# Optimization experiments

Hardware: AMD Instinct MI355X
Metric: run time of the kernel (lower is better)

## Reference

```python
import jax, jax.numpy as jnp
import numpy as np


def _combine(left, right):
    # complex mult-add combine: (a_r, x_r) o (a_l, x_l) = (a_r*a_l, a_r*x_l + x_r)
    alr, ali, xlr, xli = left
    arr, ari, xrr, xri = right
    rar = arr * alr - ari * ali
    rai = arr * ali + ari * alr
    rxr = arr * xlr - ari * xli + xrr
    rxi = arr * xli + ari * xlr + xri
    return (rar, rai, rxr, rxi)


def setup_inputs() -> dict:
    key = jax.random.key(0)
    k1, k2, k3, k4 = jax.random.split(key, 4)
    B, L, D = 8, 4096, 256
    A_re = jax.random.uniform(k1, (B, L, D), dtype=jnp.float32)  # |a|<1-ish for stability
    A_im = jax.random.normal(k2, (B, L, D), dtype=jnp.float32) * 0.1
    X_re = jax.random.normal(k3, (B, L, D), dtype=jnp.float32)
    X_im = jax.random.normal(k4, (B, L, D), dtype=jnp.float32)
    return {"A_re": A_re, "A_im": A_im, "X_re": X_re, "X_im": X_im}


def reference(A_re, A_im, X_re, X_im):
    # Inclusive scan of y_t = a_t * y_{t-1} + x_t (complex), over time axis 1.
    _, _, yr, yi = jax.lax.associative_scan(_combine, (A_re, A_im, X_re, X_im), axis=1)
    # [B, L, D, 2] real/imag stacked (equivalent of torch.view_as_real of the complex output)
    return jnp.stack([yr, yi], axis=-1)
```

## Files before the change

kernel.cpp:

```cpp
#include <hip/hip_runtime.h>

#define BATCH 8
#define SEQ   4096
#define DIM   256

typedef float floatx4 __attribute__((ext_vector_type(4)));


template <int NT, int T>
__global__ __launch_bounds__(256) void k_tile_agg(
    const float* __restrict__ Ar, const float* __restrict__ Ai,
    const float* __restrict__ Xr, const float* __restrict__ Xi,
    float4* __restrict__ agg)
{
    int wave = threadIdx.x >> 6;
    int lane = threadIdx.x & 63;
    int tile = blockIdx.x * 4 + wave;
    int b = tile / NT;
    int j = tile - b * NT;
    int d = lane * 4;

    size_t base = ((size_t)b * SEQ + (size_t)j * T) * DIM + d;

    float pr[4], pi[4], yr[4], yi[4];
#pragma unroll
    for (int k = 0; k < 4; ++k) { pr[k] = 1.f; pi[k] = 0.f; yr[k] = 0.f; yi[k] = 0.f; }

#pragma unroll 4
    for (int t = 0; t < T; ++t) {
        size_t idx = base + (size_t)t * DIM;
        float4 a_re = *(const float4*)(Ar + idx);
        float4 a_im = *(const float4*)(Ai + idx);
        float4 x_re = *(const float4*)(Xr + idx);
        float4 x_im = *(const float4*)(Xi + idx);
        const float* par = (const float*)&a_re;
        const float* pai = (const float*)&a_im;
        const float* pxr = (const float*)&x_re;
        const float* pxi = (const float*)&x_im;
#pragma unroll
        for (int k = 0; k < 4; ++k) {
            float a_r = par[k], a_i = pai[k];
            float npr = a_r * pr[k] - a_i * pi[k];
            float npi = a_r * pi[k] + a_i * pr[k];
            pr[k] = npr; pi[k] = npi;
            float nyr = a_r * yr[k] - a_i * yi[k] + pxr[k];
            float nyi = a_r * yi[k] + a_i * yr[k] + pxi[k];
            yr[k] = nyr; yi[k] = nyi;
        }
    }

    size_t o = ((size_t)b * NT + j) * DIM + d;
#pragma unroll
    for (int k = 0; k < 4; ++k)
        agg[o + k] = make_float4(pr[k], pi[k], yr[k], yi[k]);
}

template <int NT>
__global__ __launch_bounds__(256) void k_scan_agg(float4* __restrict__ agg)
{
    constexpr int NTPL = NT / 64;
    int lane = threadIdx.x & 63;
    int col  = blockIdx.x * 4 + (threadIdx.x >> 6);
    int b = col >> 8;
    int d = col & 255;

    float4 v[NTPL];
    float lar = 1.f, lai = 0.f, lxr = 0.f, lxi = 0.f;
#pragma unroll
    for (int m = 0; m < NTPL; ++m) {
        v[m] = agg[((size_t)b * NT + lane * NTPL + m) * DIM + d];
        float nar = v[m].x * lar - v[m].y * lai;
        float nai = v[m].x * lai + v[m].y * lar;
        float nxr = v[m].x * lxr - v[m].y * lxi + v[m].z;
        float nxi = v[m].x * lxi + v[m].y * lxr + v[m].w;
        lar = nar; lai = nai; lxr = nxr; lxi = nxi;
    }

    float ar = lar, ai = lai, xr = lxr, xi = lxi;
#pragma unroll
    for (int off = 1; off < 64; off <<= 1) {
        float par = __shfl_up(ar, (unsigned)off, 64);
        float pai = __shfl_up(ai, (unsigned)off, 64);
        float pxr = __shfl_up(xr, (unsigned)off, 64);
        float pxi = __shfl_up(xi, (unsigned)off, 64);
        if (lane >= off) {
            float nar = ar * par - ai * pai;
            float nai = ar * pai + ai * par;
            float nxr = ar * pxr - ai * pxi + xr;
            float nxi = ar * pxi + ai * pxr + xi;
            ar = nar; ai = nai; xr = nxr; xi = nxi;
        }
    }

    float ear = __shfl_up(ar, 1u, 64);
    float eai = __shfl_up(ai, 1u, 64);
    float exr = __shfl_up(xr, 1u, 64);
    float exi = __shfl_up(xi, 1u, 64);
    if (lane == 0) { ear = 1.f; eai = 0.f; exr = 0.f; exi = 0.f; }

#pragma unroll
    for (int m = 0; m < NTPL; ++m) {
        agg[((size_t)b * NT + lane * NTPL + m) * DIM + d] =
            make_float4(exr, exi, 0.f, 0.f);
        float nar = v[m].x * ear - v[m].y * eai;
        float nai = v[m].x * eai + v[m].y * ear;
        float nxr = v[m].x * exr - v[m].y * exi + v[m].z;
        float nxi = v[m].x * exi + v[m].y * exr + v[m].w;
        ear = nar; eai = nai; exr = nxr; exi = nxi;
    }
}

template <int NT, int T>
__global__ __launch_bounds__(256, 8) void k_apply(
    const float* __restrict__ Ar, const float* __restrict__ Ai,
    const float* __restrict__ Xr, const float* __restrict__ Xi,
    const float4* __restrict__ agg, float* __restrict__ outf)
{
    int half = threadIdx.x >> 7;
    int wl   = threadIdx.x & 127;
    int tile = blockIdx.x * 2 + half;
    int b = tile / NT;
    int j = tile - b * NT;
    int d = wl * 2;

    float yr[2], yi[2];
    size_t o = ((size_t)b * NT + j) * DIM + d;
    {
        float4 p0 = agg[o];
        float4 p1 = agg[o + 1];
        yr[0] = p0.x; yi[0] = p0.y;
        yr[1] = p1.x; yi[1] = p1.y;
    }

    size_t base = ((size_t)b * SEQ + (size_t)j * T) * DIM + d;

#pragma unroll
    for (int t = 0; t < T; ++t) {
        size_t idx = base + (size_t)t * DIM;
        float2 a_re = *(const float2*)(Ar + idx);
        float2 a_im = *(const float2*)(Ai + idx);
        float2 x_re = *(const float2*)(Xr + idx);
        float2 x_im = *(const float2*)(Xi + idx);
        const float* par = (const float*)&a_re;
        const float* pai = (const float*)&a_im;
        const float* pxr = (const float*)&x_re;
        const float* pxi = (const float*)&x_im;
#pragma unroll
        for (int k = 0; k < 2; ++k) {
            float nyr = par[k] * yr[k] - pai[k] * yi[k] + pxr[k];
            float nyi = par[k] * yi[k] + pai[k] * yr[k] + pxi[k];
            yr[k] = nyr; yi[k] = nyi;
        }
        floatx4 o1 = (floatx4){yr[0], yi[0], yr[1], yi[1]};
        __builtin_nontemporal_store(o1, (floatx4*)(outf + 2 * idx));
    }
}

extern "C" void kernel_launch(void* const* d_in, const int* in_sizes, int n_in,
                              void* d_out, int out_size, void* d_ws, size_t ws_size,
                              hipStream_t stream)
{
    const float* Ar = (const float*)d_in[0];
    const float* Ai = (const float*)d_in[1];
    const float* Xr = (const float*)d_in[2];
    const float* Xi = (const float*)d_in[3];
    float* outf = (float*)d_out;
    float4* agg = (float4*)d_ws;

    dim3 block(256);

    if (ws_size >= (size_t)BATCH * 256 * DIM * sizeof(float4)) {
        constexpr int NT = 256, T = SEQ / 256;
        dim3 grid1((BATCH * NT) / 4);
        dim3 grid3((BATCH * NT) / 2);
        k_tile_agg<NT, T><<<grid1, block, 0, stream>>>(Ar, Ai, Xr, Xi, agg);
        k_scan_agg<NT><<<(BATCH * DIM) / 4, block, 0, stream>>>(agg);
        k_apply<NT, T><<<grid3, block, 0, stream>>>(Ar, Ai, Xr, Xi, agg, outf);
    } else {
        constexpr int NT = 64, T = SEQ / 64;
        dim3 grid1((BATCH * NT) / 4);
        dim3 grid3((BATCH * NT) / 2);
        k_tile_agg<NT, T><<<grid1, block, 0, stream>>>(Ar, Ai, Xr, Xi, agg);
        k_scan_agg<NT><<<(BATCH * DIM) / 4, block, 0, stream>>>(agg);
        k_apply<NT, T><<<grid3, block, 0, stream>>>(Ar, Ai, Xr, Xi, agg, outf);
    }
}
```

Before: 67.90 us.

## Stage tile inputs into LDS via async global_load_lds in aggregation pass

Replaces the first-pass tile aggregation kernel with one that uses one block per tile. Each wave copies one of the four input arrays for the tile into LDS with direct global-to-LDS loads, then each thread scans one channel out of LDS. The goal is more memory-level parallelism and better coalescing in the bandwidth-bound aggregation pass. The cost is 64KB of LDS per block (T=16), which limits occupancy, plus a full barrier before any compute starts.

```diff
diff --git a/kernel.cpp b/kernel.cpp
--- a/kernel.cpp
+++ b/kernel.cpp
@@ -6,6 +6,57 @@
 
 typedef float floatx4 __attribute__((ext_vector_type(4)));
 
+
+template <int NT, int T>
+__global__ __launch_bounds__(256) void k_tile_agg_lds(
+    const float* __restrict__ Ar, const float* __restrict__ Ai,
+    const float* __restrict__ Xr, const float* __restrict__ Xi,
+    float4* __restrict__ agg)
+{
+    constexpr int TILE_FLOATS = T * DIM;
+    __shared__ float lds[4 * TILE_FLOATS];
+
+    int tile = blockIdx.x;
+    int b = tile / NT;
+    int j = tile - b * NT;
+
+    int wave = threadIdx.x >> 6;
+    int lane = threadIdx.x & 63;
+
+    size_t tile_off = ((size_t)b * SEQ + (size_t)j * T) * DIM;
+
+    const float* src = (wave == 0) ? Ar : (wave == 1) ? Ai
+                      : (wave == 2) ? Xr : Xi;
+    const float* gsrc = src + tile_off + (size_t)lane * 4;
+    float* lbase = &lds[wave * TILE_FLOATS];
+
+#pragma unroll
+    for (int s = 0; s < T; ++s) {
+        __builtin_amdgcn_global_load_lds(
+            (const __attribute__((address_space(1))) void*)(gsrc + s * DIM),
+            (__attribute__((address_space(3))) void*)(lbase + s * DIM),
+            16, 0, 0);
+    }
+    __syncthreads();
+
+    int d = threadIdx.x;
+    float pr = 1.f, pi = 0.f, yr = 0.f, yi = 0.f;
+#pragma unroll
+    for (int t = 0; t < T; ++t) {
+        float a_r = lds[0 * TILE_FLOATS + t * DIM + d];
+        float a_i = lds[1 * TILE_FLOATS + t * DIM + d];
+        float x_r = lds[2 * TILE_FLOATS + t * DIM + d];
+        float x_i = lds[3 * TILE_FLOATS + t * DIM + d];
+        float npr = a_r * pr - a_i * pi;
+        float npi = a_r * pi + a_i * pr;
+        pr = npr; pi = npi;
+        float nyr = a_r * yr - a_i * yi + x_r;
+        float nyi = a_r * yi + a_i * yr + x_i;
+        yr = nyr; yi = nyi;
+    }
+
+    agg[((size_t)b * NT + j) * DIM + d] = make_float4(pr, pi, yr, yi);
+}
 
 template <int NT, int T>
 __global__ __launch_bounds__(256) void k_tile_agg(
@@ -171,9 +222,9 @@
 
     if (ws_size >= (size_t)BATCH * 256 * DIM * sizeof(float4)) {
         constexpr int NT = 256, T = SEQ / 256;
-        dim3 grid1((BATCH * NT) / 4);
+        dim3 grid1(BATCH * NT);
         dim3 grid3((BATCH * NT) / 2);
-        k_tile_agg<NT, T><<<grid1, block, 0, stream>>>(Ar, Ai, Xr, Xi, agg);
+        k_tile_agg_lds<NT, T><<<grid1, block, 0, stream>>>(Ar, Ai, Xr, Xi, agg);
         k_scan_agg<NT><<<(BATCH * DIM) / 4, block, 0, stream>>>(agg);
         k_apply<NT, T><<<grid3, block, 0, stream>>>(Ar, Ai, Xr, Xi, agg, outf);
     } else {
```

After: 66.74 us. No clear change (-1.7%).

## Pipeline tile aggregation through LDS with double-buffered async global-to-LDS loads

Applied to the files above, without the earlier changes.

Replaces the first-pass tile aggregation kernel with a version that streams 8-timestep sub-tiles into LDS via global_load_lds, one wave per input array, double-buffered with explicit vmcnt waits and barriers. Each thread then computes the complex scan for one channel from LDS and writes an aggregate every two sub-tiles (16 steps, matching NT=256). The goal is to keep more memory requests in flight and overlap loading with the serial recurrence. In exchange it adds block-wide barriers, relies on precise vmcnt accounting, and uses 64KB of LDS per block, which limits occupancy.

```diff
diff --git a/kernel.cpp b/kernel.cpp
--- a/kernel.cpp
+++ b/kernel.cpp
@@ -6,6 +6,177 @@
 
 typedef float floatx4 __attribute__((ext_vector_type(4)));
 
+constexpr int NT_MAIN = 256;
+constexpr int T_MAIN  = SEQ / NT_MAIN;
+constexpr int TSUB    = 8;
+constexpr int SUB_FLOATS = TSUB * DIM;
+constexpr int NSUB_BLK   = 8;
+constexpr int NSUB_TOT   = BATCH * SEQ / TSUB;
+
+__global__ __launch_bounds__(256, 2) void k_tile_agg_pipe(
+    const float* __restrict__ Ar, const float* __restrict__ Ai,
+    const float* __restrict__ Xr, const float* __restrict__ Xi,
+    float4* __restrict__ agg)
+{
+    __shared__ float lds[2][4][SUB_FLOATS];
+
+    int wave = threadIdx.x >> 6, lane = threadIdx.x & 63;
+    int d = threadIdx.x;
+    const float* src = (wave == 0) ? Ar : (wave == 1) ? Ai
+                      : (wave == 2) ? Xr : Xi;
+
+    int s0 = blockIdx.x * NSUB_BLK;
+    const float* gsrc = src + (size_t)s0 * SUB_FLOATS + (size_t)lane * 4;
+
+    auto ISSUE = [&](int i) {
+        const float* g = gsrc + (size_t)i * SUB_FLOATS;
+        float* l = &lds[i & 1][wave][0];
+#pragma unroll
+        for (int r = 0; r < TSUB; ++r) {
+            __builtin_amdgcn_global_load_lds(
+                (const __attribute__((address_space(1))) void*)(g + r * DIM),
+                (__attribute__((address_space(3))) void*)(l + r * DIM),
+                16, 0, 0);
+        }
+    };
+
+    float pr = 1.f, pi = 0.f, yr = 0.f, yi = 0.f;
+
+    ISSUE(0);
+#pragma unroll 1
+    for (int i = 0; i < NSUB_BLK; ++i) {
+        if (i + 1 < NSUB_BLK) {
+            ISSUE(i + 1);
+            asm volatile("s_waitcnt vmcnt(8)" ::: "memory");
+        } else {
+            asm volatile("s_waitcnt vmcnt(0)" ::: "memory");
+        }
+        __builtin_amdgcn_s_barrier();
+        __builtin_amdgcn_sched_barrier(0);
+
+        const int buf = i & 1;
+#pragma unroll
+        for (int t = 0; t < TSUB; ++t) {
+            float a_r = lds[buf][0][t * DIM + d];
+            float a_i = lds[buf][1][t * DIM + d];
+            float x_r = lds[buf][2][t * DIM + d];
+            float x_i = lds[buf][3][t * DIM + d];
+            float npr = a_r * pr - a_i * pi;
+            float npi = a_r * pi + a_i * pr;
+            pr = npr; pi = npi;
+            float nyr = a_r * yr - a_i * yi + x_r;
+            float nyi = a_r * yi + a_i * yr + x_i;
+            yr = nyr; yi = nyi;
+        }
+        if (i & 1) {
+            int s = s0 + i;
+            agg[(size_t)(s >> 1) * DIM + d] = make_float4(pr, pi, yr, yi);
+            pr = 1.f; pi = 0.f; yr = 0.f; yi = 0.f;
+        }
+        __builtin_amdgcn_s_barrier();
+    }
+}
+
+template <int NT>
+__global__ __launch_bounds__(256) void k_scan_agg(float4* __restrict__ agg)
+{
+    constexpr int NTPL = NT / 64;
+    int lane = threadIdx.x & 63;
+    int col  = blockIdx.x * 4 + (threadIdx.x >> 6);
+    int b = col >> 8;
+    int d = col & 255;
+
+    float4 v[NTPL];
+    float lar = 1.f, lai = 0.f, lxr = 0.f, lxi = 0.f;
+#pragma unroll
+    for (int m = 0; m < NTPL; ++m) {
+        v[m] = agg[((size_t)b * NT + lane * NTPL + m) * DIM + d];
+        float nar = v[m].x * lar - v[m].y * lai;
+        float nai = v[m].x * lai + v[m].y * lar;
+        float nxr = v[m].x * lxr - v[m].y * lxi + v[m].z;
+        float nxi = v[m].x * lxi + v[m].y * lxr + v[m].w;
+        lar = nar; lai = nai; lxr = nxr; lxi = nxi;
+    }
+
+    float ar = lar, ai = lai, xr = lxr, xi = lxi;
+#pragma unroll
+    for (int off = 1; off < 64; off <<= 1) {
+        float par = __shfl_up(ar, (unsigned)off, 64);
+        float pai = __shfl_up(ai, (unsigned)off, 64);
+        float pxr = __shfl_up(xr, (unsigned)off, 64);
+        float pxi = __shfl_up(xi, (unsigned)off, 64);
+        if (lane >= off) {
+            float nar = ar * par - ai * pai;
+            float nai = ar * pai + ai * par;
+            float nxr = ar * pxr - ai * pxi + xr;
+            float nxi = ar * pxi + ai * pxr + xi;
+            ar = nar; ai = nai; xr = nxr; xi = nxi;
+        }
+    }
+
+    float ear = __shfl_up(ar, 1u, 64);
+    float eai = __shfl_up(ai, 1u, 64);
+    float exr = __shfl_up(xr, 1u, 64);
+    float exi = __shfl_up(xi, 1u, 64);
+    if (lane == 0) { ear = 1.f; eai = 0.f; exr = 0.f; exi = 0.f; }
+
+#pragma unroll
+    for (int m = 0; m < NTPL; ++m) {
+        agg[((size_t)b * NT + lane * NTPL + m) * DIM + d] =
+            make_float4(exr, exi, 0.f, 0.f);
+        float nar = v[m].x * ear - v[m].y * eai;
+        float nai = v[m].x * eai + v[m].y * ear;
+        float nxr = v[m].x * exr - v[m].y * exi + v[m].z;
+        float nxi = v[m].x * exi + v[m].y * exr + v[m].w;
+        ear = nar; eai = nai; exr = nxr; exi = nxi;
+    }
+}
+
+template <int NT, int T>
+__global__ __launch_bounds__(256, 8) void k_apply(
+    const float* __restrict__ Ar, const float* __restrict__ Ai,
+    const float* __restrict__ Xr, const float* __restrict__ Xi,
+    const float4* __restrict__ agg, float* __restrict__ outf)
+{
+    int half = threadIdx.x >> 7;
+    int wl   = threadIdx.x & 127;
+    int tile = blockIdx.x * 2 + half;
+    int b = tile / NT;
+    int j = tile - b * NT;
+    int d = wl * 2;
+
+    float yr[2], yi[2];
+    size_t o = ((size_t)b * NT + j) * DIM + d;
+    {
+        float4 p0 = agg[o];
+        float4 p1 = agg[o + 1];
+        yr[0] = p0.x; yi[0] = p0.y;
+        yr[1] = p1.x; yi[1] = p1.y;
+    }
+
+    size_t base = ((size_t)b * SEQ + (size_t)j * T) * DIM + d;
+
+#pragma unroll
+    for (int t = 0; t < T; ++t) {
+        size_t idx = base + (size_t)t * DIM;
+        float2 a_re = *(const float2*)(Ar + idx);
+        float2 a_im = *(const float2*)(Ai + idx);
+        float2 x_re = *(const float2*)(Xr + idx);
+        float2 x_im = *(const float2*)(Xi + idx);
+        const float* par = (const float*)&a_re;
+        const float* pai = (const float*)&a_im;
+        const float* pxr = (const float*)&x_re;
+        const float* pxi = (const float*)&x_im;
+#pragma unroll
+        for (int k = 0; k < 2; ++k) {
+            float nyr = par[k] * yr[k] - pai[k] * yi[k] + pxr[k];
+            float nyi = par[k] * yi[k] + pai[k] * yr[k] + pxi[k];
+            yr[k] = nyr; yi[k] = nyi;
+        }
+        floatx4 o1 = (floatx4){yr[0], yi[0], yr[1], yi[1]};
+        __builtin_nontemporal_store(o1, (floatx4*)(outf + 2 * idx));
+    }
+}
 
 template <int NT, int T>
 __global__ __launch_bounds__(256) void k_tile_agg(
@@ -55,107 +226,6 @@
         agg[o + k] = make_float4(pr[k], pi[k], yr[k], yi[k]);
 }
 
-template <int NT>
-__global__ __launch_bounds__(256) void k_scan_agg(float4* __restrict__ agg)
-{
-    constexpr int NTPL = NT / 64;
-    int lane = threadIdx.x & 63;
-    int col  = blockIdx.x * 4 + (threadIdx.x >> 6);
-    int b = col >> 8;
-    int d = col & 255;
-
-    float4 v[NTPL];
-    float lar = 1.f, lai = 0.f, lxr = 0.f, lxi = 0.f;
-#pragma unroll
-    for (int m = 0; m < NTPL; ++m) {
-        v[m] = agg[((size_t)b * NT + lane * NTPL + m) * DIM + d];
-        float nar = v[m].x * lar - v[m].y * lai;
-        float nai = v[m].x * lai + v[m].y * lar;
-        float nxr = v[m].x * lxr - v[m].y * lxi + v[m].z;
-        float nxi = v[m].x * lxi + v[m].y * lxr + v[m].w;
-        lar = nar; lai = nai; lxr = nxr; lxi = nxi;
-    }
-
-    float ar = lar, ai = lai, xr = lxr, xi = lxi;
-#pragma unroll
-    for (int off = 1; off < 64; off <<= 1) {
-        float par = __shfl_up(ar, (unsigned)off, 64);
-        float pai = __shfl_up(ai, (unsigned)off, 64);
-        float pxr = __shfl_up(xr, (unsigned)off, 64);
-        float pxi = __shfl_up(xi, (unsigned)off, 64);
-        if (lane >= off) {
-            float nar = ar * par - ai * pai;
-            float nai = ar * pai + ai * par;
-            float nxr = ar * pxr - ai * pxi + xr;
-            float nxi = ar * pxi + ai * pxr + xi;
-            ar = nar; ai = nai; xr = nxr; xi = nxi;
-        }
-    }
-
-    float ear = __shfl_up(ar, 1u, 64);
-    float eai = __shfl_up(ai, 1u, 64);
-    float exr = __shfl_up(xr, 1u, 64);
-    float exi = __shfl_up(xi, 1u, 64);
-    if (lane == 0) { ear = 1.f; eai = 0.f; exr = 0.f; exi = 0.f; }
-
-#pragma unroll
-    for (int m = 0; m < NTPL; ++m) {
-        agg[((size_t)b * NT + lane * NTPL + m) * DIM + d] =
-            make_float4(exr, exi, 0.f, 0.f);
-        float nar = v[m].x * ear - v[m].y * eai;
-        float nai = v[m].x * eai + v[m].y * ear;
-        float nxr = v[m].x * exr - v[m].y * exi + v[m].z;
-        float nxi = v[m].x * exi + v[m].y * exr + v[m].w;
-        ear = nar; eai = nai; exr = nxr; exi = nxi;
-    }
-}
-
-template <int NT, int T>
-__global__ __launch_bounds__(256, 8) void k_apply(
-    const float* __restrict__ Ar, const float* __restrict__ Ai,
-    const float* __restrict__ Xr, const float* __restrict__ Xi,
-    const float4* __restrict__ agg, float* __restrict__ outf)
-{
-    int half = threadIdx.x >> 7;
-    int wl   = threadIdx.x & 127;
-    int tile = blockIdx.x * 2 + half;
-    int b = tile / NT;
-    int j = tile - b * NT;
-    int d = wl * 2;
-
-    float yr[2], yi[2];
-    size_t o = ((size_t)b * NT + j) * DIM + d;
-    {
-        float4 p0 = agg[o];
-        float4 p1 = agg[o + 1];
-        yr[0] = p0.x; yi[0] = p0.y;
-        yr[1] = p1.x; yi[1] = p1.y;
-    }
-
-    size_t base = ((size_t)b * SEQ + (size_t)j * T) * DIM + d;
-
-#pragma unroll
-    for (int t = 0; t < T; ++t) {
-        size_t idx = base + (size_t)t * DIM;
-        float2 a_re = *(const float2*)(Ar + idx);
-        float2 a_im = *(const float2*)(Ai + idx);
-        float2 x_re = *(const float2*)(Xr + idx);
-        float2 x_im = *(const float2*)(Xi + idx);
-        const float* par = (const float*)&a_re;
-        const float* pai = (const float*)&a_im;
-        const float* pxr = (const float*)&x_re;
-        const float* pxi = (const float*)&x_im;
-#pragma unroll
-        for (int k = 0; k < 2; ++k) {
-            float nyr = par[k] * yr[k] - pai[k] * yi[k] + pxr[k];
-            float nyi = par[k] * yi[k] + pai[k] * yr[k] + pxi[k];
-            yr[k] = nyr; yi[k] = nyi;
-        }
-        floatx4 o1 = (floatx4){yr[0], yi[0], yr[1], yi[1]};
-        __builtin_nontemporal_store(o1, (floatx4*)(outf + 2 * idx));
-    }
-}
-
 extern "C" void kernel_launch(void* const* d_in, const int* in_sizes, int n_in,
                               void* d_out, int out_size, void* d_ws, size_t ws_size,
                               hipStream_t stream)
@@ -169,11 +239,11 @@
 
     dim3 block(256);
 
-    if (ws_size >= (size_t)BATCH * 256 * DIM * sizeof(float4)) {
-        constexpr int NT = 256, T = SEQ / 256;
-        dim3 grid1((BATCH * NT) / 4);
+    if (ws_size >= (size_t)BATCH * NT_MAIN * DIM * sizeof(float4)) {
+        constexpr int NT = NT_MAIN, T = T_MAIN;
+        dim3 gridP(NSUB_TOT / NSUB_BLK);
         dim3 grid3((BATCH * NT) / 2);
-        k_tile_agg<NT, T><<<grid1, block, 0, stream>>>(Ar, Ai, Xr, Xi, agg);
+        k_tile_agg_pipe<<<gridP, block, 0, stream>>>(Ar, Ai, Xr, Xi, agg);
         k_scan_agg<NT><<<(BATCH * DIM) / 4, block, 0, stream>>>(agg);
         k_apply<NT, T><<<grid3, block, 0, stream>>>(Ar, Ai, Xr, Xi, agg, outf);
     } else {
```

Result: faster. 65.88 us (-3.0%).

## Fuse three-kernel chunked scan into single kernel with flag-based decoupled lookback

Applied to the files above, without the earlier changes.

Replaces the tile-aggregate, aggregate-scan and apply kernels with one fused kernel. Each block computes two tile aggregates, publishes them to global memory with release flags, spin-waits on predecessor flags, then serially combines all earlier tile aggregates and re-reads its inputs to produce outputs. This removes two kernel launches and the global aggregate scan pass, but the serial lookback over up to 62 tiles and the spin-waits depend on earlier blocks being scheduled first. The fallback path also drops the nontemporal store hint.

```diff
diff --git a/kernel.cpp b/kernel.cpp
--- a/kernel.cpp
+++ b/kernel.cpp
@@ -7,8 +7,153 @@
 typedef float floatx4 __attribute__((ext_vector_type(4)));
 
 
+constexpr int NT_F   = 64;
+constexpr int T_F    = SEQ / NT_F;
+constexpr int NTILES_F = BATCH * NT_F;
+constexpr size_t VAGG_OFF = 4096;
+constexpr size_t WS_NEED_F = VAGG_OFF + (size_t)NTILES_F * DIM * 16;
+
+__device__ __forceinline__ unsigned long long pack2f(float a, float b) {
+    union { float f[2]; unsigned long long u; } u_;
+    u_.f[0] = a; u_.f[1] = b; return u_.u;
+}
+__device__ __forceinline__ void unpack2f(unsigned long long u, float& a, float& b) {
+    union { unsigned long long u; float f[2]; } u_;
+    u_.u = u; a = u_.f[0]; b = u_.f[1];
+}
+
+__global__ __launch_bounds__(256) void k_fused(
+    const float* __restrict__ Ar, const float* __restrict__ Ai,
+    const float* __restrict__ Xr, const float* __restrict__ Xi,
+    float* __restrict__ outf,
+    unsigned* __restrict__ flags, unsigned long long* __restrict__ vagg)
+{
+    __shared__ float4 s_ag[128][2];
+    constexpr int NT = NT_F, T = T_F;
+
+    int half = threadIdx.x >> 7;
+    int wl   = threadIdx.x & 127;
+    int tile = blockIdx.x * 2 + half;
+    int b  = tile / NT;
+    int j  = tile - b * NT;
+    int j0 = j & ~1;
+    int d0 = wl * 2;
+
+    size_t base = ((size_t)b * SEQ + (size_t)j * T) * DIM + d0;
+
+    float pr[2], pi[2], yr[2], yi[2];
+#pragma unroll
+    for (int c = 0; c < 2; ++c) { pr[c] = 1.f; pi[c] = 0.f; yr[c] = 0.f; yi[c] = 0.f; }
+
+#pragma unroll 4
+    for (int t = 0; t < T; ++t) {
+        size_t idx = base + (size_t)t * DIM;
+        float2 a_re = *(const float2*)(Ar + idx);
+        float2 a_im = *(const float2*)(Ai + idx);
+        float2 x_re = *(const float2*)(Xr + idx);
+        float2 x_im = *(const float2*)(Xi + idx);
+        const float* par = (const float*)&a_re;
+        const float* pai = (const float*)&a_im;
+        const float* pxr = (const float*)&x_re;
+        const float* pxi = (const float*)&x_im;
+#pragma unroll
+        for (int c = 0; c < 2; ++c) {
+            float a_r = par[c], a_i = pai[c];
+            float npr = a_r * pr[c] - a_i * pi[c];
+            float npi = a_r * pi[c] + a_i * pr[c];
+            pr[c] = npr; pi[c] = npi;
+            float nyr = a_r * yr[c] - a_i * yi[c] + pxr[c];
+            float nyi = a_r * yi[c] + a_i * yr[c] + pxi[c];
+            yr[c] = nyr; yi[c] = nyi;
+        }
+    }
+
+#pragma unroll
+    for (int c = 0; c < 2; ++c) {
+        size_t vs = 2 * ((size_t)tile * DIM + d0 + c);
+        __hip_atomic_store(&vagg[vs + 0], pack2f(pr[c], pi[c]),
+                           __ATOMIC_RELAXED, __HIP_MEMORY_SCOPE_AGENT);
+        __hip_atomic_store(&vagg[vs + 1], pack2f(yr[c], yi[c]),
+                           __ATOMIC_RELAXED, __HIP_MEMORY_SCOPE_AGENT);
+    }
+    if (half == 0) {
+        s_ag[wl][0] = make_float4(pr[0], pi[0], yr[0], yi[0]);
+        s_ag[wl][1] = make_float4(pr[1], pi[1], yr[1], yi[1]);
+    }
+    __threadfence();
+    __syncthreads();
+    if (threadIdx.x == 0) {
+        __hip_atomic_store(&flags[tile],     1u, __ATOMIC_RELEASE, __HIP_MEMORY_SCOPE_AGENT);
+        __hip_atomic_store(&flags[tile + 1], 1u, __ATOMIC_RELEASE, __HIP_MEMORY_SCOPE_AGENT);
+    }
+
+    if (threadIdx.x == 0) {
+        for (int k = 0; k < j0; ++k) {
+            while (__hip_atomic_load(&flags[b * NT + k], __ATOMIC_ACQUIRE,
+                                     __HIP_MEMORY_SCOPE_AGENT) == 0u)
+                __builtin_amdgcn_s_sleep(1);
+        }
+    }
+    __syncthreads();
+
+    float car[2], cai[2], cxr[2], cxi[2];
+#pragma unroll
+    for (int c = 0; c < 2; ++c) { car[c] = 1.f; cai[c] = 0.f; cxr[c] = 0.f; cxi[c] = 0.f; }
+
+    for (int k = 0; k < j0; ++k) {
+#pragma unroll
+        for (int c = 0; c < 2; ++c) {
+            size_t ps = 2 * ((size_t)(b * NT + k) * DIM + d0 + c);
+            unsigned long long w0 = __hip_atomic_load(&vagg[ps + 0], __ATOMIC_RELAXED, __HIP_MEMORY_SCOPE_AGENT);
+            unsigned long long w1 = __hip_atomic_load(&vagg[ps + 1], __ATOMIC_RELAXED, __HIP_MEMORY_SCOPE_AGENT);
+            float ar_, ai_, xr_, xi_;
+            unpack2f(w0, ar_, ai_);
+            unpack2f(w1, xr_, xi_);
+            float nar = ar_ * car[c] - ai_ * cai[c];
+            float nai = ar_ * cai[c] + ai_ * car[c];
+            float nxr = ar_ * cxr[c] - ai_ * cxi[c] + xr_;
+            float nxi = ar_ * cxi[c] + ai_ * cxr[c] + xi_;
+            car[c] = nar; cai[c] = nai; cxr[c] = nxr; cxi[c] = nxi;
+        }
+    }
+    if (half == 1) {
+#pragma unroll
+        for (int c = 0; c < 2; ++c) {
+            float4 v = s_ag[wl][c];
+            float nar = v.x * car[c] - v.y * cai[c];
+            float nai = v.x * cai[c] + v.y * car[c];
+            float nxr = v.x * cxr[c] - v.y * cxi[c] + v.z;
+            float nxi = v.x * cxi[c] + v.y * cxr[c] + v.w;
+            car[c] = nar; cai[c] = nai; cxr[c] = nxr; cxi[c] = nxi;
+        }
+    }
+
+    float fy_r[2] = {cxr[0], cxr[1]};
+    float fy_i[2] = {cxi[0], cxi[1]};
+#pragma unroll 4
+    for (int t = 0; t < T; ++t) {
+        size_t idx = base + (size_t)t * DIM;
+        float2 a_re = *(const float2*)(Ar + idx);
+        float2 a_im = *(const float2*)(Ai + idx);
+        float2 x_re = *(const float2*)(Xr + idx);
+        float2 x_im = *(const float2*)(Xi + idx);
+        const float* par = (const float*)&a_re;
+        const float* pai = (const float*)&a_im;
+        const float* pxr = (const float*)&x_re;
+        const float* pxi = (const float*)&x_im;
+#pragma unroll
+        for (int c = 0; c < 2; ++c) {
+            float nyr = par[c] * fy_r[c] - pai[c] * fy_i[c] + pxr[c];
+            float nyi = par[c] * fy_i[c] + pai[c] * fy_r[c] + pxi[c];
+            fy_r[c] = nyr; fy_i[c] = nyi;
+        }
+        *(float4*)(outf + 2 * idx) =
+            make_float4(fy_r[0], fy_i[0], fy_r[1], fy_i[1]);
+    }
+}
+
 template <int NT, int T>
-__global__ __launch_bounds__(256) void k_tile_agg(
+__global__ __launch_bounds__(256) void k_tile_agg_fb(
     const float* __restrict__ Ar, const float* __restrict__ Ai,
     const float* __restrict__ Xr, const float* __restrict__ Xi,
     float4* __restrict__ agg)
@@ -56,7 +201,7 @@
 }
 
 template <int NT>
-__global__ __launch_bounds__(256) void k_scan_agg(float4* __restrict__ agg)
+__global__ __launch_bounds__(256) void k_scan_agg_fb(float4* __restrict__ agg)
 {
     constexpr int NTPL = NT / 64;
     int lane = threadIdx.x & 63;
@@ -111,7 +256,7 @@
 }
 
 template <int NT, int T>
-__global__ __launch_bounds__(256, 8) void k_apply(
+__global__ __launch_bounds__(256, 8) void k_apply_fb(
     const float* __restrict__ Ar, const float* __restrict__ Ai,
     const float* __restrict__ Xr, const float* __restrict__ Xi,
     const float4* __restrict__ agg, float* __restrict__ outf)
@@ -151,8 +296,7 @@
             float nyi = par[k] * yi[k] + pai[k] * yr[k] + pxi[k];
             yr[k] = nyr; yi[k] = nyi;
         }
-        floatx4 o1 = (floatx4){yr[0], yi[0], yr[1], yi[1]};
-        __builtin_nontemporal_store(o1, (floatx4*)(outf + 2 * idx));
+        *(float4*)(outf + 2 * idx) = make_float4(yr[0], yi[0], yr[1], yi[1]);
     }
 }
 
@@ -165,23 +309,20 @@
     const float* Xr = (const float*)d_in[2];
     const float* Xi = (const float*)d_in[3];
     float* outf = (float*)d_out;
-    float4* agg = (float4*)d_ws;
-
-    dim3 block(256);
-
-    if (ws_size >= (size_t)BATCH * 256 * DIM * sizeof(float4)) {
-        constexpr int NT = 256, T = SEQ / 256;
-        dim3 grid1((BATCH * NT) / 4);
-        dim3 grid3((BATCH * NT) / 2);
-        k_tile_agg<NT, T><<<grid1, block, 0, stream>>>(Ar, Ai, Xr, Xi, agg);
-        k_scan_agg<NT><<<(BATCH * DIM) / 4, block, 0, stream>>>(agg);
-        k_apply<NT, T><<<grid3, block, 0, stream>>>(Ar, Ai, Xr, Xi, agg, outf);
+
+    if (ws_size >= WS_NEED_F) {
+        unsigned* flags = (unsigned*)d_ws;
+        unsigned long long* vagg =
+            (unsigned long long*)((char*)d_ws + VAGG_OFF);
+        hipMemsetAsync(d_ws, 0, VAGG_OFF, stream);
+        k_fused<<<NTILES_F / 2, 256, 0, stream>>>(
+            Ar, Ai, Xr, Xi, outf, flags, vagg);
     } else {
+        float4* agg = (float4*)d_ws;
         constexpr int NT = 64, T = SEQ / 64;
-        dim3 grid1((BATCH * NT) / 4);
-        dim3 grid3((BATCH * NT) / 2);
-        k_tile_agg<NT, T><<<grid1, block, 0, stream>>>(Ar, Ai, Xr, Xi, agg);
-        k_scan_agg<NT><<<(BATCH * DIM) / 4, block, 0, stream>>>(agg);
-        k_apply<NT, T><<<grid3, block, 0, stream>>>(Ar, Ai, Xr, Xi, agg, outf);
-    }
-}
+        dim3 block(256);
+        k_tile_agg_fb<NT, T><<<(BATCH * NT) / 4, block, 0, stream>>>(Ar, Ai, Xr, Xi, agg);
+        k_scan_agg_fb<NT><<<(BATCH * DIM) / 4, block, 0, stream>>>(agg);
+        k_apply_fb<NT, T><<<(BATCH * NT) / 2, block, 0, stream>>>(Ar, Ai, Xr, Xi, agg, outf);
+    }
+}
```

Measured after the change: 165.9 us. 2.44x slower.
